# Kernel tuning notes

Hardware: AMD Instinct MI355X
Metric: run time of the kernel (lower is better)

The kernel has to match this reference:

```python
import jax, jax.numpy as jnp
import numpy as np

N, E, D, EDGE_DIM = 50000, 150000, 100, 200

def _w(key, fi, fo):
    return jax.random.normal(key, (fi, fo), dtype=jnp.float32) / np.float32(np.sqrt(fi))

def setup_inputs():
    key = jax.random.key(0)
    ks = jax.random.split(key, 40)
    inp = {}
    inp["x"] = jax.random.normal(ks[0], (N, D), dtype=jnp.float32)
    inp["msg"] = jax.random.normal(ks[1], (E, D), dtype=jnp.float32)
    # TimeEncoder: Linear(1, D)
    inp["time_w"] = _w(ks[2], 1, D)
    inp["time_b"] = jnp.zeros((D,), jnp.float32)
    # TransformerConv 1: in=100, heads=8, out=100, concat -> 800
    H1 = 8 * D
    inp["c1_qw"] = _w(ks[3], D, H1); inp["c1_qb"] = jnp.zeros((H1,), jnp.float32)
    inp["c1_kw"] = _w(ks[4], D, H1); inp["c1_kb"] = jnp.zeros((H1,), jnp.float32)
    inp["c1_vw"] = _w(ks[5], D, H1); inp["c1_vb"] = jnp.zeros((H1,), jnp.float32)
    inp["c1_ew"] = _w(ks[6], EDGE_DIM, H1)  # lin_edge has no bias in PyG
    inp["c1_sw"] = _w(ks[7], D, H1); inp["c1_sb"] = jnp.zeros((H1,), jnp.float32)
    # TransformerConv 2: in=800, heads=1, out=100, concat=False
    inp["c2_qw"] = _w(ks[8], H1, D); inp["c2_qb"] = jnp.zeros((D,), jnp.float32)
    inp["c2_kw"] = _w(ks[9], H1, D); inp["c2_kb"] = jnp.zeros((D,), jnp.float32)
    inp["c2_vw"] = _w(ks[10], H1, D); inp["c2_vb"] = jnp.zeros((D,), jnp.float32)
    inp["c2_ew"] = _w(ks[11], EDGE_DIM, D)
    inp["c2_sw"] = _w(ks[12], H1, D); inp["c2_sb"] = jnp.zeros((D,), jnp.float32)
    # LinkPredictor (in_channels=100, out=2)
    inp["lp_src_w"] = _w(ks[13], D, 2 * D); inp["lp_src_b"] = jnp.zeros((2 * D,), jnp.float32)
    inp["lp_dst_w"] = _w(ks[14], D, 2 * D); inp["lp_dst_b"] = jnp.zeros((2 * D,), jnp.float32)
    inp["lp1_w"] = _w(ks[15], 4 * D, 8 * D); inp["lp1_b"] = jnp.zeros((8 * D,), jnp.float32)
    inp["lp2_w"] = _w(ks[16], 8 * D, 2 * D); inp["lp2_b"] = jnp.zeros((2 * D,), jnp.float32)
    inp["lp3_w"] = _w(ks[17], 2 * D, D // 2); inp["lp3_b"] = jnp.zeros((D // 2,), jnp.float32)
    inp["lp4_w"] = _w(ks[18], D // 2, 2); inp["lp4_b"] = jnp.zeros((2,), jnp.float32)
    inp["last_update"] = jax.random.randint(ks[19], (N,), 0, 1000000)
    inp["t"] = jax.random.randint(ks[20], (E,), 0, 1000000)
    inp["edge_index"] = jax.random.randint(ks[21], (2, E), 0, N)
    return inp

def _tconv(x, src, dst, edge_attr, qw, qb, kw, kb, vw, vb, ew, sw, sb, heads, out_ch, concat, n):
    q = (x @ qw + qb).reshape(n, heads, out_ch)
    k = (x @ kw + kb).reshape(n, heads, out_ch)
    v = (x @ vw + vb).reshape(n, heads, out_ch)
    e = (edge_attr @ ew).reshape(-1, heads, out_ch)        # [E,H,C]
    kj = k[src] + e                                        # gather src keys + edge
    alpha = jnp.sum(q[dst] * kj, axis=-1) / np.float32(np.sqrt(out_ch))  # [E,H]
    amax = jax.ops.segment_max(alpha, dst, num_segments=n)
    ex = jnp.exp(alpha - amax[dst])
    denom = jax.ops.segment_sum(ex, dst, num_segments=n)
    a = ex / (denom[dst] + 1e-16)                          # per-dest softmax
    agg = jax.ops.segment_sum((v[src] + e) * a[..., None], dst, num_segments=n)
    out = agg.reshape(n, heads * out_ch) if concat else jnp.mean(agg, axis=1)
    return out + x @ sw + sb                               # root/skip connection

def reference(x, msg, time_w, time_b,
              c1_qw, c1_qb, c1_kw, c1_kb, c1_vw, c1_vb, c1_ew, c1_sw, c1_sb,
              c2_qw, c2_qb, c2_kw, c2_kb, c2_vw, c2_vb, c2_ew, c2_sw, c2_sb,
              lp_src_w, lp_src_b, lp_dst_w, lp_dst_b,
              lp1_w, lp1_b, lp2_w, lp2_b, lp3_w, lp3_b, lp4_w, lp4_b,
              last_update, t, edge_index):
    src, dst = edge_index[0], edge_index[1]
    rel_t = (last_update[src] - t).astype(jnp.float32)[:, None]  # [E,1]
    rel_enc = jnp.cos(rel_t @ time_w + time_b)                   # [E,D]
    edge_attr = jnp.concatenate([rel_enc, msg], axis=-1)         # [E,200]
    h = jax.nn.relu(_tconv(x, src, dst, edge_attr, c1_qw, c1_qb, c1_kw, c1_kb,
                           c1_vw, c1_vb, c1_ew, c1_sw, c1_sb, 8, D, True, N))
    h = jax.nn.relu(_tconv(h, src, dst, edge_attr, c2_qw, c2_qb, c2_kw, c2_kb,
                           c2_vw, c2_vb, c2_ew, c2_sw, c2_sb, 1, D, False, N))
    hh = jnp.concatenate([h[src] @ lp_src_w + lp_src_b,
                          h[dst] @ lp_dst_w + lp_dst_b], axis=-1)
    hh = jnp.tanh(hh @ lp1_w + lp1_b)
    hh = jnp.tanh(hh @ lp2_w + lp2_b)
    hh = jnp.tanh(hh @ lp3_w + lp3_b)
    return hh @ lp4_w + lp4_b
```

## Files before the change

kernel.cpp:

```cpp
#include <hip/hip_runtime.h>
#include <hip/hip_bf16.h>
#include <math.h>

typedef __hip_bfloat16 bf16;
typedef short s16x8 __attribute__((ext_vector_type(8)));
typedef float f32x4 __attribute__((ext_vector_type(4)));

#define NN 50000
#define EE 150000
#define EH 75000

static __device__ __forceinline__ float b2f(bf16 x){ return __bfloat162float(x); }
static __device__ __forceinline__ bf16 f2b(float x){ return __float2bfloat16(x); }
static __device__ __forceinline__ short f2s(float x){
  union { bf16 b; short s; } u; u.b = f2b(x); return u.s;
}
static __device__ __forceinline__ float u2f_lo(unsigned u){ union{unsigned i;float f;}c; c.i=u<<16; return c.f; }
static __device__ __forceinline__ float u2f_hi(unsigned u){ union{unsigned i;float f;}c; c.i=u&0xffff0000u; return c.f; }

static __device__ __forceinline__ float fast_tanh(float x){
  float a = fabsf(x);
  float e = __expf(2.0f*a);
  float t = 1.0f - __fdividef(2.0f, e + 1.0f);
  return x < 0.f ? -t : t;
}

static __device__ __forceinline__ void gload_lds16(const void* g, void* l){
  __builtin_amdgcn_global_load_lds((const __attribute__((address_space(1))) void*)g,
                                   (__attribute__((address_space(3))) void*)l, 16, 0, 0);
}

template<int N> static __device__ __forceinline__ void wait_vmcnt(){
  if constexpr(N==0) asm volatile("s_waitcnt vmcnt(0)" ::: "memory");
  else if constexpr(N==1) asm volatile("s_waitcnt vmcnt(1)" ::: "memory");
  else if constexpr(N==2) asm volatile("s_waitcnt vmcnt(2)" ::: "memory");
  else if constexpr(N==3) asm volatile("s_waitcnt vmcnt(3)" ::: "memory");
  else if constexpr(N==4) asm volatile("s_waitcnt vmcnt(4)" ::: "memory");
  else if constexpr(N==5) asm volatile("s_waitcnt vmcnt(5)" ::: "memory");
  else asm volatile("s_waitcnt vmcnt(6)" ::: "memory");
}
static __device__ __forceinline__ void wait_lgkm0(){
  asm volatile("s_waitcnt lgkmcnt(0)" ::: "memory");
}
static __device__ __forceinline__ void memfence(){
  asm volatile("" ::: "memory");
}

__global__ void k_zero(int* __restrict__ p, int n){
  int i = blockIdx.x*blockDim.x + threadIdx.x;
  if(i<n) p[i]=0;
}

__global__ void k_hist(const int* __restrict__ dst, int* __restrict__ deg){
  int i = blockIdx.x*blockDim.x + threadIdx.x;
  if(i<EE) atomicAdd(&deg[dst[i]], 1);
}

__global__ void k_scan(const int* __restrict__ deg, int* __restrict__ rowptr){
  __shared__ int part[1024];
  int tid = threadIdx.x;
  const int n = NN;
  int chunk = (n + 1023)/1024;
  int start = tid*chunk;
  int end = start + chunk; if(end > n) end = n;
  int s = 0;
  for(int i=start;i<end;i++) s += deg[i];
  part[tid] = s; __syncthreads();
  for(int off=1; off<1024; off<<=1){
    int v = (tid>=off)? part[tid-off] : 0;
    __syncthreads();
    part[tid] += v;
    __syncthreads();
  }
  int run = (tid==0)? 0 : part[tid-1];
  for(int i=start;i<end;i++){ rowptr[i]=run; run += deg[i]; }
  if(tid==0) rowptr[n] = part[1023];
}

__global__ void k_scatter(const int* __restrict__ dst, const int* __restrict__ srcv,
                          const int* __restrict__ rowptr,
                          int* __restrict__ cursor, int* __restrict__ elist,
                          int* __restrict__ ssrc){
  int e = blockIdx.x*blockDim.x + threadIdx.x;
  if(e<EE){
    int d=dst[e]; int p=atomicAdd(&cursor[d],1);
    int pos = rowptr[d]+p;
    elist[pos]=e; ssrc[pos]=srcv[e];
  }
}

__global__ void k_relenc(const int* __restrict__ elist, const int* __restrict__ ssrc,
                         const int* __restrict__ tt, const int* __restrict__ lu,
                         const float* __restrict__ tw, const float* __restrict__ tb,
                         bf16* __restrict__ rel){
  int i = blockIdx.x*blockDim.x + threadIdx.x;
  if(i >= EE*112) return;
  int j = i/112, c = i - j*112;
  float v = 0.f;
  if(c < 100){
    int e = elist[j];
    float rt  = (float)(lu[ssrc[j]] - tt[e]);
    float arg = __fadd_rn(__fmul_rn(rt, tw[c]), tb[c]);
    v = cosf(arg);
  }
  rel[i] = f2b(v);
}

__global__ void k_cvtpad(const float* __restrict__ in, int incols,
                         bf16* __restrict__ outp, int outcols, int total){
  int i = blockIdx.x*blockDim.x + threadIdx.x;
  if(i >= total) return;
  int r = i/outcols, c = i - r*outcols;
  outp[i] = f2b(c < incols ? in[(size_t)r*incols + c] : 0.f);
}

__global__ void k_wt2(const float* __restrict__ W, int K, int N, int colofs, int ncols,
                      bf16* __restrict__ WT, int kpad, int nrows){
  int i = blockIdx.x*blockDim.x + threadIdx.x;
  if(i >= nrows*kpad) return;
  int n = i / kpad, k = i - n*kpad;
  float v = (n<ncols && k<K)? W[(size_t)k*N + colofs + n] : 0.f;
  WT[i] = f2b(v);
}

__global__ void k_wtc1(const float* __restrict__ qw, const float* __restrict__ kw,
                       const float* __restrict__ vw, bf16* __restrict__ outp){
  int i = blockIdx.x*blockDim.x + threadIdx.x;
  if(i >= 8*320*128) return;
  int h = i/(320*128), r = (i/128)%320, k = i&127;
  float v = 0.f;
  if(r < 300 && k < 100){
    int s = r/100, n = r - s*100;
    const float* W = s==0? qw : s==1? kw : vw;
    v = W[(size_t)k*800 + h*100 + n];
  }
  outp[i] = f2b(v);
}

__global__ void k_wte(const float* __restrict__ ew, int N, int colofs,
                      bf16* __restrict__ outp){
  int i = blockIdx.x*blockDim.x + threadIdx.x;
  if(i >= 112*256) return;
  int r = i>>8, k = i&255;
  float v = 0.f;
  if(r < 100){
    if(k < 100) v = ew[(size_t)k*N + colofs + r];
    else if(k >= 128 && k < 228) v = ew[(size_t)(k-28)*N + colofs + r];
  }
  outp[i] = f2b(v);
}

__global__ void k_bstack3(const float* __restrict__ b0, const float* __restrict__ b1,
                          const float* __restrict__ b2, int W, int H,
                          float* __restrict__ outp){
  int i = blockIdx.x*blockDim.x + threadIdx.x;
  if(i >= H*3*W) return;
  int h = i/(3*W), r = i - h*3*W, s = r/W, c = r - s*W;
  const float* b = s==0? b0 : s==1? b1 : b2;
  outp[i] = b[h*W + c];
}

__global__ void k_foldw(const float* __restrict__ sw, const float* __restrict__ dw,
                        const float* __restrict__ w1, bf16* __restrict__ o){
  int i = blockIdx.x*blockDim.x + threadIdx.x;
  if(i >= 800*224) return;
  int n = i/224, k = i - n*224;
  float s = 0.f;
  if(k < 100){
    for(int j=0;j<200;j++) s += sw[k*200+j]*w1[(size_t)j*800+n];
  } else if(k >= 112 && k < 212){
    int kk = k-112;
    for(int j=0;j<200;j++) s += dw[kk*200+j]*w1[(size_t)(200+j)*800+n];
  }
  o[i] = f2b(s);
}
__global__ void k_foldb(const float* __restrict__ sb, const float* __restrict__ db,
                        const float* __restrict__ w1, const float* __restrict__ b1,
                        float* __restrict__ o){
  int n = blockIdx.x*blockDim.x + threadIdx.x;
  if(n >= 800) return;
  float s = b1[n];
  for(int j=0;j<200;j++) s += sb[j]*w1[(size_t)j*800+n] + db[j]*w1[(size_t)(200+j)*800+n];
  o[n] = s;
}

template<int NT>
static __device__ void mm_body(
    char* lds, int bx, int nstrip,
    const bf16* __restrict__ A1, int lda1, int kv1, const int* __restrict__ g1,
    int KS,
    const bf16* __restrict__ A2b, int lda2b, int kv2b, const int* __restrict__ g2,
    const float* __restrict__ A2f, int lda2f, int kv2f,
    const bf16* __restrict__ WT, int kpad,
    const bf16* __restrict__ zbuf,
    const float* __restrict__ bias,
    bf16* __restrict__ C, int ldc,
    int M, int nvalid, int act)
{
  constexpr int BN = NT*16;
  constexpr int BPASS = (BN*4 + 255)/256;
  constexpr int ABYTES = 8192;
  constexpr int BUFSZ = ABYTES + BPASS*4096;

  const int tid  = threadIdx.x;
  const int wave = tid>>6, lane = tid&63;
  const int quad = lane>>4, lo = lane&15;
  WT += (size_t)nstrip*BN*kpad;
  C  += (size_t)nstrip*BN;
  if(bias) bias += nstrip*BN;
  const int nval = nvalid - nstrip*BN;
  const int row0 = bx*128;

  float bvr[NT];
#pragma unroll
  for(int n=0;n<NT;n++){
    int col = n*16 + lo;
    bvr[n] = (bias && col < nval) ? bias[col] : 0.f;
  }
#pragma unroll
  for(int n=0;n<NT;n++) asm volatile("" :: "v"(bvr[n]));

  const char*  a1b[2];
  const char*  a2bp[2];
  const float* f2base[2];
  int acol0[2];
#pragma unroll
  for(int p=0;p<2;p++){
    int s = p*256 + tid;
    int row = s>>2, cp = s&3;
    int q = cp ^ ((row>>1)&3);
    int col0 = q*8;
    int rg = row0 + row; if(rg > M-1) rg = M-1;
    int r1 = g1 ? g1[rg] : rg;
    int r2 = g2 ? g2[rg] : rg;
    acol0[p] = col0;
    a1b[p]   = (const char*)A1 + ((size_t)r1*lda1 + col0)*2;
    a2bp[p]  = A2b ? (const char*)A2b + ((size_t)r2*lda2b)*2 : nullptr;
    f2base[p]= A2f ? (A2f + (size_t)r2*lda2f) : nullptr;
  }
  const char* bbase[BPASS];
#pragma unroll
  for(int p=0;p<BPASS;p++){
    int s = p*256 + tid;
    int rb = s>>2; if(rb > BN-1) rb = BN-1;
    int cp = s&3;
    int lq = cp ^ ((rb>>1)&3);
    bbase[p] = (const char*)WT + ((size_t)rb*kpad + lq*8)*2;
  }

  f32x4 acc[2][NT];
#pragma unroll
  for(int m=0;m<2;m++)
#pragma unroll
    for(int n=0;n<NT;n++) acc[m][n] = (f32x4){0.f,0.f,0.f,0.f};

  float4 pf0[2], pf1[2];

  auto stageA1 = [&](char* buf, int kb){
#pragma unroll
    for(int p=0;p<2;p++){
      int k = kb + acol0[p];
      const char* s;
      if(k < KS) s = (k < kv1) ? (a1b[p] + (size_t)kb*2) : (const char*)zbuf;
      else { int o = k - KS; s = (o < kv2b) ? (a2bp[p] + (size_t)o*2) : (const char*)zbuf; }
      gload_lds16(s, buf + p*4096 + wave*1024);
    }
  };
  auto loadA2f = [&](int kb){
#pragma unroll
    for(int p=0;p<2;p++){
      int o = kb + acol0[p] - KS;
      const float* ap = f2base[p] + o;
      pf0[p] = (o   < kv2f) ? *(const float4*)ap     : (float4){0.f,0.f,0.f,0.f};
      pf1[p] = (o+4 < kv2f) ? *(const float4*)(ap+4) : (float4){0.f,0.f,0.f,0.f};
    }
  };
  auto writeA2 = [&](char* buf){
#pragma unroll
    for(int p=0;p<2;p++){
      s16x8 v;
      v[0]=f2s(pf0[p].x); v[1]=f2s(pf0[p].y); v[2]=f2s(pf0[p].z); v[3]=f2s(pf0[p].w);
      v[4]=f2s(pf1[p].x); v[5]=f2s(pf1[p].y); v[6]=f2s(pf1[p].z); v[7]=f2s(pf1[p].w);
      *(s16x8*)(buf + p*4096 + (size_t)tid*16) = v;
    }
  };
  auto stageB = [&](char* buf, int kb){
#pragma unroll
    for(int p=0;p<BPASS;p++)
      gload_lds16(bbase[p] + (size_t)kb*2, buf + ABYTES + p*4096 + wave*1024);
  };
  auto compute = [&](const char* buf){
    s16x8 af[2];
#pragma unroll
    for(int m=0;m<2;m++){
      int rl = wave*32 + m*16 + lo;
      int cp = quad ^ ((rl>>1)&3);
      af[m] = *(const s16x8*)(buf + rl*64 + cp*16);
    }
#pragma unroll
    for(int n=0;n<NT;n++){
      int rb = n*16 + lo;
      int cp = quad ^ ((rb>>1)&3);
      s16x8 bfr = *(const s16x8*)(buf + ABYTES + rb*64 + cp*16);
      acc[0][n] = __builtin_amdgcn_mfma_f32_16x16x32_bf16(af[0], bfr, acc[0][n], 0,0,0);
      acc[1][n] = __builtin_amdgcn_mfma_f32_16x16x32_bf16(af[1], bfr, acc[1][n], 0,0,0);
    }
  };

  const int T = kpad >> 5;
  stageA1(lds, 0); stageB(lds, 0);
  if(T > 1){ stageA1(lds + BUFSZ, 32); stageB(lds + BUFSZ, 32); }

  for(int t=0; t<T; t++){
    bool nb  = (t+1 < T);
    bool nfp = nb && A2f && (((t+1)<<5) >= KS);
    if(!nb)      wait_vmcnt<0>();
    else if(nfp) wait_vmcnt<BPASS>();
    else         wait_vmcnt<2+BPASS>();
    wait_lgkm0();
    __builtin_amdgcn_s_barrier();
    memfence();
    int tp = t+2;
    bool sp  = (tp < T);
    bool spf = sp && A2f && ((tp<<5) >= KS);
    char* nb3 = lds + (tp%3)*BUFSZ;
    if(sp){
      int kb2 = tp<<5;
      if(spf) loadA2f(kb2);
      else    stageA1(nb3, kb2);
      stageB(nb3, kb2);
    }
    compute(lds + (t%3)*BUFSZ);
    if(spf) writeA2(nb3);
  }

  const int r0 = (lane&1)<<1;
#pragma unroll
  for(int n=0;n<NT;n++){
    int col  = n*16 + lo;
    int pcol = col & ~1;
    bool cok = (pcol < nval);
    float bv = bvr[n];
#pragma unroll
    for(int m=0;m<2;m++){
      float v[4];
#pragma unroll
      for(int r=0;r<4;r++){
        float t = acc[m][n][r] + bv;
        if(act==1) t = fmaxf(t, 0.f);
        else if(act==2) t = fast_tanh(t);
        v[r] = t;
      }
      unsigned mylo = (unsigned)(unsigned short)f2s(v[r0])
                    | ((unsigned)(unsigned short)f2s(v[r0+1])<<16);
      unsigned snd  = (unsigned)(unsigned short)f2s(v[r0^2])
                    | ((unsigned)(unsigned short)f2s(v[(r0^2)+1])<<16);
      unsigned got  = (unsigned)__shfl_xor((int)snd, 1);
      unsigned w0, w1;
      if(lane&1){ w0 = (got & 0xffffu) | (mylo<<16); w1 = (got>>16) | (mylo & 0xffff0000u); }
      else      { w0 = (mylo & 0xffffu) | (got<<16); w1 = (mylo>>16) | (got & 0xffff0000u); }
      if(cok){
        int prow = row0 + wave*32 + m*16 + quad*4 + r0;
        if(prow   < M) *(unsigned*)(C + (size_t)prow*ldc + pcol) = w0;
        if(prow+1 < M) *(unsigned*)(C + (size_t)(prow+1)*ldc + pcol) = w1;
      }
    }
  }
}

template<int NT>
__global__ __launch_bounds__(256) void mm_tile(
    const bf16* A1, int lda1, int kv1, const int* g1, int KS,
    const bf16* A2b, int lda2b, int kv2b, const int* g2,
    const float* A2f, int lda2f, int kv2f,
    const bf16* WT, int kpad, const bf16* zbuf, const float* bias,
    bf16* C, int ldc, int M, int nvalid, int act)
{
  constexpr int BUFSZ = 8192 + ((NT*16*4+255)/256)*4096;
  __shared__ __align__(16) char lds[3*BUFSZ];
  mm_body<NT>(lds, blockIdx.x, blockIdx.y, A1,lda1,kv1,g1, KS,
              A2b,lda2b,kv2b,g2, A2f,lda2f,kv2f, WT,kpad, zbuf, bias,
              C,ldc, M,nvalid,act);
}

template<int NT>
__global__ __launch_bounds__(256) void mm_gath(
    const bf16* __restrict__ A, int lda, int KS,
    const int* __restrict__ gs, const int* __restrict__ gd,
    const bf16* __restrict__ WT,
    const float* __restrict__ bias,
    bf16* __restrict__ C, int ldc,
    int M, int nvalid, int act)
{
  constexpr int T = 7;
  constexpr int KPAD = 224;
  constexpr int BN = NT*16;
  constexpr int BPASS = (BN*4 + 255)/256;
  constexpr int BUFSZ = BPASS*4096;
  __shared__ __align__(16) char lds[3*BUFSZ];

  const int tid  = threadIdx.x;
  const int wave = tid>>6, lane = tid&63;
  const int quad = lane>>4, lo = lane&15;
  const int nstrip = blockIdx.y;
  const bf16* WTs = WT + (size_t)nstrip*BN*KPAD;
  C += (size_t)nstrip*BN;
  const float* bp = bias ? bias + nstrip*BN : nullptr;
  const int nval = nvalid - nstrip*BN;
  const int row0 = blockIdx.x*128;

  float bvr[NT];
#pragma unroll
  for(int n=0;n<NT;n++){
    int col = n*16 + lo;
    bvr[n] = (bp && col < nval) ? bp[col] : 0.f;
  }

  const bf16* abase[2][2];
#pragma unroll
  for(int m=0;m<2;m++){
    int r = row0 + wave*32 + m*16 + lo; if(r > M-1) r = M-1;
    abase[m][0] = A + (size_t)gs[r]*lda;
    abase[m][1] = A + (size_t)gd[r]*lda;
  }

  s16x8 areg[T][2];
#pragma unroll
  for(int t=0;t<T;t++){
#pragma unroll
    for(int m=0;m<2;m++){
      int k = t*32 + quad*8;
      const bf16* p = (k < KS) ? (abase[m][0] + k) : (abase[m][1] + (k - KS));
      asm volatile("global_load_dwordx4 %0, %1, off"
                   : "=v"(areg[t][m]) : "v"(p));
    }
  }
  memfence();

  const char* bbase[BPASS];
#pragma unroll
  for(int p=0;p<BPASS;p++){
    int s = p*256 + tid;
    int rb = s>>2; if(rb > BN-1) rb = BN-1;
    int cp = s&3;
    int lq = cp ^ ((rb>>1)&3);
    bbase[p] = (const char*)WTs + ((size_t)rb*KPAD + lq*8)*2;
  }
  auto stageB = [&](char* buf, int kb){
#pragma unroll
    for(int p=0;p<BPASS;p++)
      gload_lds16(bbase[p] + (size_t)kb*2, buf + p*4096 + wave*1024);
  };

  f32x4 acc[2][NT];
#pragma unroll
  for(int m=0;m<2;m++)
#pragma unroll
    for(int n=0;n<NT;n++) acc[m][n] = (f32x4){0.f,0.f,0.f,0.f};

  stageB(lds, 0);
  stageB(lds + BUFSZ, 32);

#pragma unroll
  for(int t=0; t<T; t++){
    if(t < T-1) wait_vmcnt<BPASS>();
    else        wait_vmcnt<0>();
    wait_lgkm0();
    __builtin_amdgcn_s_barrier();
    memfence();
    if(t+2 < T) stageB(lds + ((t+2)%3)*BUFSZ, (t+2)*32);
    const char* buf = lds + (t%3)*BUFSZ;
#pragma unroll
    for(int n=0;n<NT;n++){
      int rb = n*16 + lo;
      int cp = quad ^ ((rb>>1)&3);
      s16x8 bfr = *(const s16x8*)(buf + rb*64 + cp*16);
      acc[0][n] = __builtin_amdgcn_mfma_f32_16x16x32_bf16(areg[t][0], bfr, acc[0][n], 0,0,0);
      acc[1][n] = __builtin_amdgcn_mfma_f32_16x16x32_bf16(areg[t][1], bfr, acc[1][n], 0,0,0);
    }
  }

  const int r0 = (lane&1)<<1;
#pragma unroll
  for(int n=0;n<NT;n++){
    int col  = n*16 + lo;
    int pcol = col & ~1;
    bool cok = (pcol < nval);
    float bv = bvr[n];
#pragma unroll
    for(int m=0;m<2;m++){
      float v[4];
#pragma unroll
      for(int r=0;r<4;r++){
        float t = acc[m][n][r] + bv;
        if(act==1) t = fmaxf(t, 0.f);
        else if(act==2) t = fast_tanh(t);
        v[r] = t;
      }
      unsigned mylo = (unsigned)(unsigned short)f2s(v[r0])
                    | ((unsigned)(unsigned short)f2s(v[r0+1])<<16);
      unsigned snd  = (unsigned)(unsigned short)f2s(v[r0^2])
                    | ((unsigned)(unsigned short)f2s(v[(r0^2)+1])<<16);
      unsigned got  = (unsigned)__shfl_xor((int)snd, 1);
      unsigned w0, w1;
      if(lane&1){ w0 = (got & 0xffffu) | (mylo<<16); w1 = (got>>16) | (mylo & 0xffff0000u); }
      else      { w0 = (mylo & 0xffffu) | (got<<16); w1 = (mylo>>16) | (got & 0xffff0000u); }
      if(cok){
        int prow = row0 + wave*32 + m*16 + quad*4 + r0;
        if(prow   < M) *(unsigned*)(C + (size_t)prow*ldc + pcol) = w0;
        if(prow+1 < M) *(unsigned*)(C + (size_t)(prow+1)*ldc + pcol) = w1;
      }
    }
  }
}

__global__ __launch_bounds__(256) void mm_edge(
    const bf16* __restrict__ relc,
    const float* __restrict__ msg,
    const int* __restrict__ elist,
    const bf16* __restrict__ WT,
    bf16* __restrict__ C, int ldc,
    int M)
{
  constexpr int NT = 7;
  constexpr int BN = 112;
  constexpr int BPASS = 2;
  constexpr int KPAD = 256, T = 8;
  constexpr int BUFSZ = BPASS*4096;
  __shared__ __align__(16) char lds[3*BUFSZ];

  const int tid  = threadIdx.x;
  const int wave = tid>>6, lane = tid&63;
  const int quad = lane>>4, lo = lane&15;
  const int row0 = blockIdx.x*128;

  const bf16*  arel[2];
  const float* amsg[2];
#pragma unroll
  for(int m=0;m<2;m++){
    int r = row0 + wave*32 + m*16 + lo; if(r > M-1) r = M-1;
    arel[m] = relc + (size_t)r*112;
    amsg[m] = msg + (size_t)elist[r]*100;
  }

  s16x8 ar[4][2];
#pragma unroll
  for(int t=0;t<4;t++){
#pragma unroll
    for(int m=0;m<2;m++){
      int k = t*32 + quad*8;
      int kc = (k < 112) ? k : 96;
      ar[t][m] = *(const s16x8*)(arel[m] + kc);
    }
  }
  float4 mf0[4][2], mf1[4][2];
#pragma unroll
  for(int t=0;t<4;t++){
#pragma unroll
    for(int m=0;m<2;m++){
      int mk = t*32 + quad*8;
      mf0[t][m] = (mk   < 100) ? *(const float4*)(amsg[m] + mk)   : (float4){0.f,0.f,0.f,0.f};
      mf1[t][m] = (mk+4 < 100) ? *(const float4*)(amsg[m] + mk+4) : (float4){0.f,0.f,0.f,0.f};
    }
  }
  memfence();

  const char* bbase[BPASS];
#pragma unroll
  for(int p=0;p<BPASS;p++){
    int s = p*256 + tid;
    int rb = s>>2; if(rb > BN-1) rb = BN-1;
    int cp = s&3;
    int lq = cp ^ ((rb>>1)&3);
    bbase[p] = (const char*)WT + ((size_t)rb*KPAD + lq*8)*2;
  }
  auto stageB = [&](char* buf, int kb){
#pragma unroll
    for(int p=0;p<BPASS;p++)
      gload_lds16(bbase[p] + (size_t)kb*2, buf + p*4096 + wave*1024);
  };

  f32x4 acc[2][NT];
#pragma unroll
  for(int m=0;m<2;m++)
#pragma unroll
    for(int n=0;n<NT;n++) acc[m][n] = (f32x4){0.f,0.f,0.f,0.f};

  stageB(lds, 0);
  stageB(lds + BUFSZ, 32);

#pragma unroll
  for(int t=0; t<T; t++){
    if(t < T-1) wait_vmcnt<BPASS>();
    else        wait_vmcnt<0>();
    wait_lgkm0();
    __builtin_amdgcn_s_barrier();
    memfence();
    if(t+2 < T) stageB(lds + ((t+2)%3)*BUFSZ, (t+2)*32);
    const char* buf = lds + (t%3)*BUFSZ;
    s16x8 af[2];
    if(t < 4){
#pragma unroll
      for(int m=0;m<2;m++) af[m] = ar[t][m];
    } else {
#pragma unroll
      for(int m=0;m<2;m++){
        float4 f0 = mf0[t-4][m], f1 = mf1[t-4][m];
        s16x8 v;
        v[0]=f2s(f0.x); v[1]=f2s(f0.y); v[2]=f2s(f0.z); v[3]=f2s(f0.w);
        v[4]=f2s(f1.x); v[5]=f2s(f1.y); v[6]=f2s(f1.z); v[7]=f2s(f1.w);
        af[m] = v;
      }
    }
#pragma unroll
    for(int n=0;n<NT;n++){
      int rb = n*16 + lo;
      int cp = quad ^ ((rb>>1)&3);
      s16x8 bfr = *(const s16x8*)(buf + rb*64 + cp*16);
      acc[0][n] = __builtin_amdgcn_mfma_f32_16x16x32_bf16(af[0], bfr, acc[0][n], 0,0,0);
      acc[1][n] = __builtin_amdgcn_mfma_f32_16x16x32_bf16(af[1], bfr, acc[1][n], 0,0,0);
    }
  }

  const int r0 = (lane&1)<<1;
#pragma unroll
  for(int n=0;n<NT;n++){
    int col  = n*16 + lo;
    int pcol = col & ~1;
    bool cok = (pcol < 100);
#pragma unroll
    for(int m=0;m<2;m++){
      float v[4];
#pragma unroll
      for(int r=0;r<4;r++) v[r] = acc[m][n][r];
      unsigned mylo = (unsigned)(unsigned short)f2s(v[r0])
                    | ((unsigned)(unsigned short)f2s(v[r0+1])<<16);
      unsigned snd  = (unsigned)(unsigned short)f2s(v[r0^2])
                    | ((unsigned)(unsigned short)f2s(v[(r0^2)+1])<<16);
      unsigned got  = (unsigned)__shfl_xor((int)snd, 1);
      unsigned w0, w1;
      if(lane&1){ w0 = (got & 0xffffu) | (mylo<<16); w1 = (got>>16) | (mylo & 0xffff0000u); }
      else      { w0 = (mylo & 0xffffu) | (got<<16); w1 = (mylo>>16) | (got & 0xffff0000u); }
      if(cok){
        int prow = row0 + wave*32 + m*16 + quad*4 + r0;
        if(prow   < M) *(unsigned*)(C + (size_t)prow*ldc + pcol) = w0;
        if(prow+1 < M) *(unsigned*)(C + (size_t)(prow+1)*ldc + pcol) = w1;
      }
    }
  }
}

__global__ __launch_bounds__(256) void k_attn(
    const int* __restrict__ rowptr, const int* __restrict__ ssrc,
    const bf16* __restrict__ qkv, const bf16* __restrict__ ehc,
    bf16* __restrict__ hout, int ldh, int colofs, int zpad)
{
  int wave = threadIdx.x>>6, lane = threadIdx.x&63;
  int node = blockIdx.x*4 + wave;
  if(node >= NN) return;
  bool act = (lane < 50);
  float q0=0.f, q1=0.f;
  const unsigned* qrow = (const unsigned*)(qkv + (size_t)node*300);
  if(act){ unsigned u = qrow[lane]; q0=u2f_lo(u); q1=u2f_hi(u); }
  int s0 = rowptr[node], s1 = rowptr[node+1];
  float m = -3.4e38f, d = 0.f, a0 = 0.f, a1 = 0.f;
  for(int j=s0; j<s1; j++){
    int sn = ssrc[j];
    float p = 0.f, e0=0.f, e1=0.f;
    if(act){
      unsigned uk = ((const unsigned*)(qkv + (size_t)sn*300 + 100))[lane];
      unsigned ue = ((const unsigned*)(ehc + (size_t)j*100))[lane];
      e0=u2f_lo(ue); e1=u2f_hi(ue);
      p = q0*(u2f_lo(uk)+e0) + q1*(u2f_hi(uk)+e1);
    }
    for(int off=32; off; off>>=1) p += __shfl_xor(p, off);
    float alpha = p * 0.1f;
    float mn = fmaxf(m, alpha);
    float sc = __expf(m - mn);
    float wv = __expf(alpha - mn);
    d = d*sc + wv;
    if(act){
      unsigned uv = ((const unsigned*)(qkv + (size_t)sn*300 + 200))[lane];
      a0 = a0*sc + wv*(u2f_lo(uv)+e0);
      a1 = a1*sc + wv*(u2f_hi(uv)+e1);
    }
    m = mn;
  }
  if(act){
    float inv = 1.f/(d + 1e-16f);
    unsigned us = ((const unsigned*)(hout + (size_t)node*ldh + colofs))[lane];
    float h0 = fmaxf(u2f_lo(us) + a0*inv, 0.f);
    float h1 = fmaxf(u2f_hi(us) + a1*inv, 0.f);
    bf16* op = hout + (size_t)node*ldh + colofs + lane*2;
    op[0] = f2b(h0); op[1] = f2b(h1);
  } else if(zpad && lane < 56){
    bf16* op = hout + (size_t)node*ldh + colofs + lane*2;
    op[0] = f2b(0.f); op[1] = f2b(0.f);
  }
}

__global__ void k_lpout(const bf16* __restrict__ t3, const float* __restrict__ w4,
                        const float* __restrict__ b4, float* __restrict__ out,
                        int base, int n){
  int i = blockIdx.x*blockDim.x + threadIdx.x;
  if(i >= n*2) return;
  int g = i>>1, j = i&1;
  const bf16* tp = t3 + (size_t)g*50;
  float s = 0.f;
  for(int k=0;k<50;k++) s += b2f(tp[k])*w4[k*2+j];
  out[(size_t)(base+g)*2 + j] = s + b4[j];
}

extern "C" void kernel_launch(void* const* d_in, const int* in_sizes, int n_in,
                              void* d_out, int out_size, void* d_ws, size_t ws_size,
                              hipStream_t stream){
  const float* x       = (const float*)d_in[0];
  const float* msg     = (const float*)d_in[1];
  const float* time_w  = (const float*)d_in[2];
  const float* time_b  = (const float*)d_in[3];
  const float* c1_qw=(const float*)d_in[4];  const float* c1_qb=(const float*)d_in[5];
  const float* c1_kw=(const float*)d_in[6];  const float* c1_kb=(const float*)d_in[7];
  const float* c1_vw=(const float*)d_in[8];  const float* c1_vb=(const float*)d_in[9];
  const float* c1_ew=(const float*)d_in[10];
  const float* c1_sw=(const float*)d_in[11]; const float* c1_sb=(const float*)d_in[12];
  const float* c2_qw=(const float*)d_in[13]; const float* c2_qb=(const float*)d_in[14];
  const float* c2_kw=(const float*)d_in[15]; const float* c2_kb=(const float*)d_in[16];
  const float* c2_vw=(const float*)d_in[17]; const float* c2_vb=(const float*)d_in[18];
  const float* c2_ew=(const float*)d_in[19];
  const float* c2_sw=(const float*)d_in[20]; const float* c2_sb=(const float*)d_in[21];
  const float* lp_src_w=(const float*)d_in[22]; const float* lp_src_b=(const float*)d_in[23];
  const float* lp_dst_w=(const float*)d_in[24]; const float* lp_dst_b=(const float*)d_in[25];
  const float* lp1_w=(const float*)d_in[26]; const float* lp1_b=(const float*)d_in[27];
  const float* lp2_w=(const float*)d_in[28]; const float* lp2_b=(const float*)d_in[29];
  const float* lp3_w=(const float*)d_in[30]; const float* lp3_b=(const float*)d_in[31];
  const float* lp4_w=(const float*)d_in[32]; const float* lp4_b=(const float*)d_in[33];
  const int* last_update=(const int*)d_in[34];
  const int* tt =(const int*)d_in[35];
  const int* edge_index=(const int*)d_in[36];
  const int* src = edge_index;
  const int* dst = edge_index + EE;
  float* out = (float*)d_out;

  char* ws = (char*)d_ws;
  bf16*  h1    = (bf16*) (ws + 0);
  bf16*  relc  = (bf16*) (ws + 80000000);
  bf16*  ehc   = (bf16*) (ws + 113600000);
  bf16*  qkv   = (bf16*) (ws + 143600000);
  bf16*  h2p   = (bf16*) (ws + 183600000);
  bf16*  xb    = (bf16*) (ws + 183600000);
  int*   rowptr= (int*)  (ws + 194800000);
  int*   elist = (int*)  (ws + 195000064);
  int*   ssrc  = (int*)  (ws + 195600064);
  int*   deg   = (int*)  (ws + 196200064);
  int*   cursor= (int*)  (ws + 196400064);
  bf16* c1all  = (bf16*)(ws + 196600064);
  bf16* c1eall = (bf16*)(ws + 197255424);
  bf16* c1swt  = (bf16*)(ws + 197714176);
  bf16* c2all  = (bf16*)(ws + 197918976);
  bf16* c2swt  = (bf16*)(ws + 198430976);
  bf16* c2e    = (bf16*)(ws + 198610176);
  bf16* lp1tF  = (bf16*)(ws + 198667520);
  bf16* lp2t   = (bf16*)(ws + 199025920);
  bf16* lp3t   = (bf16*)(ws + 199384320);
  float* c1ball= (float*)(ws + 199412992);
  float* c2ball= (float*)(ws + 199422592);
  float* lp1c  = (float*)(ws + 199423808);
  bf16* zbuf   = (bf16*)(ws + 199427008);
  bf16* lt1 = (bf16*)(ws + 0);
  bf16* lt2 = (bf16*)(ws + 120000000);
  bf16* lt3 = (bf16*)(ws + 150000000);

  k_wtc1<<<(8*320*128+255)/256,256,0,stream>>>(c1_qw,c1_kw,c1_vw,c1all);
  for(int h=0; h<8; h++)
    k_wte<<<(112*256+255)/256,256,0,stream>>>(c1_ew, 800, h*100, c1eall + (size_t)h*112*256);
  k_wte<<<(112*256+255)/256,256,0,stream>>>(c2_ew, 100, 0, c2e);
  k_wt2<<<(800*128+255)/256,256,0,stream>>>(c1_sw,100,800,0,800,c1swt,128,800);
  k_wt2<<<(100*800+255)/256,256,0,stream>>>(c2_qw,800,100,0,100,c2all,         800,100);
  k_wt2<<<(100*800+255)/256,256,0,stream>>>(c2_kw,800,100,0,100,c2all+100*800, 800,100);
  k_wt2<<<(100*800+255)/256,256,0,stream>>>(c2_vw,800,100,0,100,c2all+200*800, 800,100);
  k_wt2<<<(20*800+255)/256,256,0,stream>>>(c2_qw,800,100,0,0,   c2all+300*800, 800,20);
  k_wt2<<<(112*800+255)/256,256,0,stream>>>(c2_sw,800,100,0,100,c2swt,800,112);
  k_wt2<<<(224*800+255)/256,256,0,stream>>>(lp2_w,800,200,0,200,lp2t,800,224);
  k_wt2<<<(64*224+255)/256,256,0,stream>>>(lp3_w,200,50,0,50,lp3t,224,64);
  k_foldw<<<(800*224+255)/256,256,0,stream>>>(lp_src_w, lp_dst_w, lp1_w, lp1tF);
  k_foldb<<<(800+255)/256,256,0,stream>>>(lp_src_b, lp_dst_b, lp1_w, lp1_b, lp1c);
  k_bstack3<<<(8*300+255)/256,256,0,stream>>>(c1_qb,c1_kb,c1_vb,100,8,c1ball);
  k_bstack3<<<(300+255)/256,256,0,stream>>>(c2_qb,c2_kb,c2_vb,100,1,c2ball);
  k_zero<<<1,64,0,stream>>>((int*)zbuf, 16);
  k_cvtpad<<<(NN*112+255)/256,256,0,stream>>>(x, 100, xb, 112, NN*112);

  k_zero   <<<(NN+255)/256, 256, 0, stream>>>(deg, NN);
  k_zero   <<<(NN+255)/256, 256, 0, stream>>>(cursor, NN);
  k_hist   <<<(EE+255)/256, 256, 0, stream>>>(dst, deg);
  k_scan   <<<1, 1024, 0, stream>>>(deg, rowptr);
  k_scatter<<<(EE+255)/256, 256, 0, stream>>>(dst, src, rowptr, cursor, elist, ssrc);

  k_relenc<<<(EE*112+255)/256, 256, 0, stream>>>(elist, ssrc, tt, last_update,
                                                 time_w, time_b, relc);

  int gN = (NN + 127)/128;
  int gE = (EE + 127)/128;
  int gL = (EH + 127)/128;
  int gA = (NN + 3)/4;

  mm_tile<10><<<dim3(gN,5),256,0,stream>>>(xb,112,112,nullptr, 128,
      nullptr,0,0,nullptr, nullptr,0,0,
      c1swt,128, zbuf, c1_sb, h1,800, NN,800,0);

  for(int h=0; h<8; h++){
    mm_tile<10><<<dim3(gN,2),256,0,stream>>>(xb,112,112,nullptr, 128,
        nullptr,0,0,nullptr, nullptr,0,0,
        c1all + (size_t)h*320*128, 128, zbuf, c1ball + h*300, qkv,300, NN,300,0);
    mm_edge<<<gE,256,0,stream>>>(relc, msg, elist,
        c1eall + (size_t)h*112*256, ehc,100, EE);
    k_attn<<<gA,256,0,stream>>>(rowptr, ssrc, qkv, ehc, h1, 800, h*100, 0);
  }

  mm_tile<10><<<dim3(gN,2),256,0,stream>>>(h1,800,800,nullptr, 800,
      nullptr,0,0,nullptr, nullptr,0,0,
      c2all,800, zbuf, c2ball, qkv,300, NN,300,0);
  mm_edge<<<gE,256,0,stream>>>(relc, msg, elist, c2e, ehc,100, EE);
  mm_tile<7><<<dim3(gN,1),256,0,stream>>>(h1,800,800,nullptr, 800,
      nullptr,0,0,nullptr, nullptr,0,0,
      c2swt,800, zbuf, c2_sb, h2p,112, NN,100,0);
  k_attn<<<gA,256,0,stream>>>(rowptr, ssrc, qkv, ehc, h2p, 112, 0, 1);

  for(int half=0; half<2; half++){
    const int* esrc = src + half*EH;
    const int* edst = dst + half*EH;
    mm_gath<10><<<dim3(gL,5),256,0,stream>>>(h2p,112,112, esrc, edst,
        lp1tF, lp1c, lt1,800, EH,800,2);
    mm_tile<7><<<dim3(gL,2),256,0,stream>>>(lt1,800,800,nullptr, 800,
        nullptr,0,0,nullptr, nullptr,0,0,
        lp2t,800, zbuf, lp2_b, lt2,200, EH,200,2);
    mm_tile<4><<<dim3(gL,1),256,0,stream>>>(lt2,200,200,nullptr, 224,
        nullptr,0,0,nullptr, nullptr,0,0,
        lp3t,224, zbuf, lp3_b, lt3,50, EH,50,2);
    k_lpout<<<(EH*2+255)/256,256,0,stream>>>(lt3, lp4_w, lp4_b, out, half*EH, EH);
  }

  (void)in_sizes; (void)n_in; (void)out_size; (void)ws_size;
}
```

Measured before the change: 1.931 ms.

## Loop N-strips inside gather GEMM to reuse gathered A; prefetch attention edges

The gather GEMM for the first link-predictor layer used to launch one block per N-strip, and each block re-gathered the same src/dst rows into registers. It now launches one block per row tile and loops over all five strips, so the gathered A fragments are loaded once and reused. The cost is fewer blocks and less parallelism, plus a serial loop with an extra barrier per strip. Separately, the attention kernel software-prefetches the next edge's K, edge and V values to overlap the dependent loads with the softmax math, which adds register pressure.

```diff
diff --git a/kernel.cpp b/kernel.cpp
--- a/kernel.cpp
+++ b/kernel.cpp
@@ -383,7 +383,7 @@
               C,ldc, M,nvalid,act);
 }
 
-template<int NT>
+template<int NT, int NS>
 __global__ __launch_bounds__(256) void mm_gath(
     const bf16* __restrict__ A, int lda, int KS,
     const int* __restrict__ gs, const int* __restrict__ gd,
@@ -402,19 +402,8 @@
   const int tid  = threadIdx.x;
   const int wave = tid>>6, lane = tid&63;
   const int quad = lane>>4, lo = lane&15;
-  const int nstrip = blockIdx.y;
-  const bf16* WTs = WT + (size_t)nstrip*BN*KPAD;
-  C += (size_t)nstrip*BN;
-  const float* bp = bias ? bias + nstrip*BN : nullptr;
-  const int nval = nvalid - nstrip*BN;
   const int row0 = blockIdx.x*128;
-
-  float bvr[NT];
-#pragma unroll
-  for(int n=0;n<NT;n++){
-    int col = n*16 + lo;
-    bvr[n] = (bp && col < nval) ? bp[col] : 0.f;
-  }
+  const int r0e  = (lane&1)<<1;
 
   const bf16* abase[2][2];
 #pragma unroll
@@ -423,7 +412,6 @@
     abase[m][0] = A + (size_t)gs[r]*lda;
     abase[m][1] = A + (size_t)gd[r]*lda;
   }
-
   s16x8 areg[T][2];
 #pragma unroll
   for(int t=0;t<T;t++){
@@ -437,80 +425,100 @@
   }
   memfence();
 
-  const char* bbase[BPASS];
-#pragma unroll
-  for(int p=0;p<BPASS;p++){
-    int s = p*256 + tid;
-    int rb = s>>2; if(rb > BN-1) rb = BN-1;
-    int cp = s&3;
-    int lq = cp ^ ((rb>>1)&3);
-    bbase[p] = (const char*)WTs + ((size_t)rb*KPAD + lq*8)*2;
-  }
-  auto stageB = [&](char* buf, int kb){
-#pragma unroll
-    for(int p=0;p<BPASS;p++)
-      gload_lds16(bbase[p] + (size_t)kb*2, buf + p*4096 + wave*1024);
-  };
-
   f32x4 acc[2][NT];
-#pragma unroll
-  for(int m=0;m<2;m++)
-#pragma unroll
-    for(int n=0;n<NT;n++) acc[m][n] = (f32x4){0.f,0.f,0.f,0.f};
-
-  stageB(lds, 0);
-  stageB(lds + BUFSZ, 32);
-
-#pragma unroll
-  for(int t=0; t<T; t++){
-    if(t < T-1) wait_vmcnt<BPASS>();
-    else        wait_vmcnt<0>();
-    wait_lgkm0();
+
+#pragma unroll 1
+  for(int s=0; s<NS; s++){
+    const bf16* WTs = WT + (size_t)s*BN*KPAD;
+    bf16* Cs = C + s*BN;
+    const int nval = nvalid - s*BN;
+
+    float bvr[NT];
+#pragma unroll
+    for(int n=0;n<NT;n++){
+      int col = n*16 + lo;
+      bvr[n] = (bias && col < nval) ? bias[s*BN + col] : 0.f;
+    }
+#pragma unroll
+    for(int n=0;n<NT;n++) asm volatile("" :: "v"(bvr[n]));
+    memfence();
+
+    const char* bbase[BPASS];
+#pragma unroll
+    for(int p=0;p<BPASS;p++){
+      int ss = p*256 + tid;
+      int rb = ss>>2; if(rb > BN-1) rb = BN-1;
+      int cp = ss&3;
+      int lq = cp ^ ((rb>>1)&3);
+      bbase[p] = (const char*)WTs + ((size_t)rb*KPAD + lq*8)*2;
+    }
+    auto stageB = [&](char* buf, int kb){
+#pragma unroll
+      for(int p=0;p<BPASS;p++)
+        gload_lds16(bbase[p] + (size_t)kb*2, buf + p*4096 + wave*1024);
+    };
+
+#pragma unroll
+    for(int m=0;m<2;m++)
+#pragma unroll
+      for(int n=0;n<NT;n++) acc[m][n] = (f32x4){0.f,0.f,0.f,0.f};
+
+    stageB(lds, 0);
+    stageB(lds + BUFSZ, 32);
+
+#pragma unroll
+    for(int t=0; t<T; t++){
+      if(t < T-1) wait_vmcnt<BPASS>();
+      else        wait_vmcnt<0>();
+      wait_lgkm0();
+      __builtin_amdgcn_s_barrier();
+      memfence();
+      if(t+2 < T) stageB(lds + ((t+2)%3)*BUFSZ, (t+2)*32);
+      const char* buf = lds + (t%3)*BUFSZ;
+#pragma unroll
+      for(int n=0;n<NT;n++){
+        int rb = n*16 + lo;
+        int cp = quad ^ ((rb>>1)&3);
+        s16x8 bfr = *(const s16x8*)(buf + rb*64 + cp*16);
+        acc[0][n] = __builtin_amdgcn_mfma_f32_16x16x32_bf16(areg[t][0], bfr, acc[0][n], 0,0,0);
+        acc[1][n] = __builtin_amdgcn_mfma_f32_16x16x32_bf16(areg[t][1], bfr, acc[1][n], 0,0,0);
+      }
+    }
+
+#pragma unroll
+    for(int n=0;n<NT;n++){
+      int col  = n*16 + lo;
+      int pcol = col & ~1;
+      bool cok = (pcol < nval);
+      float bv = bvr[n];
+#pragma unroll
+      for(int m=0;m<2;m++){
+        float v[4];
+#pragma unroll
+        for(int r=0;r<4;r++){
+          float t = acc[m][n][r] + bv;
+          if(act==1) t = fmaxf(t, 0.f);
+          else if(act==2) t = fast_tanh(t);
+          v[r] = t;
+        }
+        unsigned mylo = (unsigned)(unsigned short)f2s(v[r0e])
+                      | ((unsigned)(unsigned short)f2s(v[r0e+1])<<16);
+        unsigned snd  = (unsigned)(unsigned short)f2s(v[r0e^2])
+                      | ((unsigned)(unsigned short)f2s(v[(r0e^2)+1])<<16);
+        unsigned got  = (unsigned)__shfl_xor((int)snd, 1);
+        unsigned w0, w1;
+        if(lane&1){ w0 = (got & 0xffffu) | (mylo<<16); w1 = (got>>16) | (mylo & 0xffff0000u); }
+        else      { w0 = (mylo & 0xffffu) | (got<<16); w1 = (mylo>>16) | (got & 0xffff0000u); }
+        if(cok){
+          int prow = row0 + wave*32 + m*16 + quad*4 + r0e;
+          if(prow   < M) *(unsigned*)(Cs + (size_t)prow*ldc + pcol) = w0;
+          if(prow+1 < M) *(unsigned*)(Cs + (size_t)(prow+1)*ldc + pcol) = w1;
+        }
+      }
+    }
+    wait_vmcnt<0>();
     __builtin_amdgcn_s_barrier();
     memfence();
-    if(t+2 < T) stageB(lds + ((t+2)%3)*BUFSZ, (t+2)*32);
-    const char* buf = lds + (t%3)*BUFSZ;
-#pragma unroll
-    for(int n=0;n<NT;n++){
-      int rb = n*16 + lo;
-      int cp = quad ^ ((rb>>1)&3);
-      s16x8 bfr = *(const s16x8*)(buf + rb*64 + cp*16);
-      acc[0][n] = __builtin_amdgcn_mfma_f32_16x16x32_bf16(areg[t][0], bfr, acc[0][n], 0,0,0);
-      acc[1][n] = __builtin_amdgcn_mfma_f32_16x16x32_bf16(areg[t][1], bfr, acc[1][n], 0,0,0);
-    }
-  }
-
-  const int r0 = (lane&1)<<1;
-#pragma unroll
-  for(int n=0;n<NT;n++){
-    int col  = n*16 + lo;
-    int pcol = col & ~1;
-    bool cok = (pcol < nval);
-    float bv = bvr[n];
-#pragma unroll
-    for(int m=0;m<2;m++){
-      float v[4];
-#pragma unroll
-      for(int r=0;r<4;r++){
-        float t = acc[m][n][r] + bv;
-        if(act==1) t = fmaxf(t, 0.f);
-        else if(act==2) t = fast_tanh(t);
-        v[r] = t;
-      }
-      unsigned mylo = (unsigned)(unsigned short)f2s(v[r0])
-                    | ((unsigned)(unsigned short)f2s(v[r0+1])<<16);
-      unsigned snd  = (unsigned)(unsigned short)f2s(v[r0^2])
-                    | ((unsigned)(unsigned short)f2s(v[(r0^2)+1])<<16);
-      unsigned got  = (unsigned)__shfl_xor((int)snd, 1);
-      unsigned w0, w1;
-      if(lane&1){ w0 = (got & 0xffffu) | (mylo<<16); w1 = (got>>16) | (mylo & 0xffff0000u); }
-      else      { w0 = (mylo & 0xffffu) | (got<<16); w1 = (mylo>>16) | (got & 0xffff0000u); }
-      if(cok){
-        int prow = row0 + wave*32 + m*16 + quad*4 + r0;
-        if(prow   < M) *(unsigned*)(C + (size_t)prow*ldc + pcol) = w0;
-        if(prow+1 < M) *(unsigned*)(C + (size_t)(prow+1)*ldc + pcol) = w1;
-      }
-    }
   }
 }
 
@@ -664,14 +672,30 @@
   if(act){ unsigned u = qrow[lane]; q0=u2f_lo(u); q1=u2f_hi(u); }
   int s0 = rowptr[node], s1 = rowptr[node+1];
   float m = -3.4e38f, d = 0.f, a0 = 0.f, a1 = 0.f;
+  unsigned uk=0, ue=0, uv=0;
+  if(s0 < s1){
+    int sn = ssrc[s0];
+    if(act){
+      uk = ((const unsigned*)(qkv + (size_t)sn*300 + 100))[lane];
+      ue = ((const unsigned*)(ehc + (size_t)s0*100))[lane];
+      uv = ((const unsigned*)(qkv + (size_t)sn*300 + 200))[lane];
+    }
+  }
   for(int j=s0; j<s1; j++){
-    int sn = ssrc[j];
+    unsigned cuk=uk, cue=ue, cuv=uv;
+    int nj = j+1;
+    if(nj < s1){
+      int sn2 = ssrc[nj];
+      if(act){
+        uk = ((const unsigned*)(qkv + (size_t)sn2*300 + 100))[lane];
+        ue = ((const unsigned*)(ehc + (size_t)nj*100))[lane];
+        uv = ((const unsigned*)(qkv + (size_t)sn2*300 + 200))[lane];
+      }
+    }
     float p = 0.f, e0=0.f, e1=0.f;
     if(act){
-      unsigned uk = ((const unsigned*)(qkv + (size_t)sn*300 + 100))[lane];
-      unsigned ue = ((const unsigned*)(ehc + (size_t)j*100))[lane];
-      e0=u2f_lo(ue); e1=u2f_hi(ue);
-      p = q0*(u2f_lo(uk)+e0) + q1*(u2f_hi(uk)+e1);
+      e0=u2f_lo(cue); e1=u2f_hi(cue);
+      p = q0*(u2f_lo(cuk)+e0) + q1*(u2f_hi(cuk)+e1);
     }
     for(int off=32; off; off>>=1) p += __shfl_xor(p, off);
     float alpha = p * 0.1f;
@@ -680,9 +704,8 @@
     float wv = __expf(alpha - mn);
     d = d*sc + wv;
     if(act){
-      unsigned uv = ((const unsigned*)(qkv + (size_t)sn*300 + 200))[lane];
-      a0 = a0*sc + wv*(u2f_lo(uv)+e0);
-      a1 = a1*sc + wv*(u2f_hi(uv)+e1);
+      a0 = a0*sc + wv*(u2f_lo(cuv)+e0);
+      a1 = a1*sc + wv*(u2f_hi(cuv)+e1);
     }
     m = mn;
   }
@@ -828,7 +851,7 @@
   for(int half=0; half<2; half++){
     const int* esrc = src + half*EH;
     const int* edst = dst + half*EH;
-    mm_gath<10><<<dim3(gL,5),256,0,stream>>>(h2p,112,112, esrc, edst,
+    mm_gath<10,5><<<gL,256,0,stream>>>(h2p,112,112, esrc, edst,
         lp1tF, lp1c, lt1,800, EH,800,2);
     mm_tile<7><<<dim3(gL,2),256,0,stream>>>(lt1,800,800,nullptr, 800,
         nullptr,0,0,nullptr, nullptr,0,0,
```

Result: slower. 1.977 ms (+2.4%).
